# Optimization experiments

Hardware: AMD Instinct MI355X
Metric: run time of the kernel (lower is better)

The kernel has to match this reference:

```python
import jax, jax.numpy as jnp
import numpy as np

# binactive: sign() forward, straight-through (hardtanh) backward, matching the CUDA kernel
@jax.custom_vjp
def binactive(x):
    return jnp.sign(x)

def _binactive_fwd(x):
    return jnp.sign(x), x

def _binactive_bwd(x, g):
    return (g * (jnp.abs(x) <= 1.0).astype(g.dtype),)

binactive.defvjp(_binactive_fwd, _binactive_bwd)

B, C_IN, C_OUT, K, H, W = 32, 256, 256, 3, 56, 56

def setup_inputs() -> dict:
    key = jax.random.key(0)
    k1, k2, k3 = jax.random.split(key, 3)
    x = jax.random.normal(k1, (B, C_IN, H, W), dtype=jnp.float32)
    n = C_IN * (K ^ 2)  # faithful to the (buggy) `kernel_size ^ 2` in reset_parameters
    stdv = 1.0 / np.sqrt(n)
    weight = jax.random.uniform(k2, (C_OUT, C_IN, K, K), dtype=jnp.float32, minval=-stdv, maxval=stdv)
    mask = jax.random.uniform(k3, (C_OUT, 1, 1, 1), dtype=jnp.float32, minval=-1e-4, maxval=1e-4)
    return {"x": x, "weight": weight, "mask": mask}

def reference(x, weight, mask):
    xb = binactive(x)                      # sign-binarized activations, [B,Cin,H,W]
    fm = (binactive(mask) - 1.0) / 2.0     # binact=True branch: 0 if mask>0, -1 if mask<0
    w = weight * fm + weight               # per-output-filter gating of weights
    out = jax.lax.conv_general_dilated(
        xb, w,
        window_strides=(1, 1),
        padding=((1, 1), (1, 1)),
        dimension_numbers=("NCHW", "OIHW", "NCHW"),
    )
    return out  # [B, Cout, H, W]
```

## Files before the change

kernel.cpp:

```cpp
#include <hip/hip_runtime.h>

#define B_    32
#define CIN   256
#define COUT  256
#define Hh    56
#define Ww    56
#define HP    58
#define WP    58
#define Kk    2304
#define NT    18

#define QSCALE 2016.0f
#define QINV   (1.0f/2016.0f)

#define XPAD_BYTES ((size_t)B_*HP*WP*CIN)
#define XPAD_GUARD 16384
#define AWT_OFF    (XPAD_BYTES + XPAD_GUARD)
#define AWT_BYTES  ((size_t)NT*32768)
#define META_OFF   (AWT_OFF + AWT_BYTES)
#define WS_REQUIRED (META_OFF + 1040)

#define LDS_TOTAL 90112
#define TP 260

typedef __attribute__((ext_vector_type(4))) int i32x4;

__device__ __forceinline__ void gload_lds16(const void* g, void* l) {
  __builtin_amdgcn_global_load_lds(
      (const __attribute__((address_space(1))) unsigned int*)g,
      (__attribute__((address_space(3))) unsigned int*)l, 16, 0, 0);
}

__global__ __launch_bounds__(256) void prep_all(
    const float* __restrict__ x,
    const float* __restrict__ wgt,
    const float* __restrict__ mask,
    int* __restrict__ meta,
    signed char* __restrict__ awt,
    signed char* __restrict__ xp) {
  const int t = threadIdx.x;
  const int bid = blockIdx.x;
  if (bid < HP * B_) {
    const int hp = bid % HP, b = bid / HP;
    unsigned* orow = (unsigned*)(xp + (size_t)(b * HP + hp) * WP * CIN);
    if (hp == 0 || hp == HP - 1) {
      for (int i = t; i < WP * CIN / 4; i += 256) orow[i] = 0u;
      return;
    }
    __shared__ __align__(16) signed char tile[WP * TP];
    const int h = hp - 1;
    tile[t] = 0;
    tile[(WP - 1) * TP + t] = 0;
    const int tx = t & 63, ty = t >> 6;
    if (tx < Ww) {
      const float* xr = x + ((size_t)b * CIN * Hh + h) * Ww;
      for (int ci0 = ty * 4; ci0 < CIN; ci0 += 16) {
        unsigned pk = 0;
        #pragma unroll
        for (int j = 0; j < 4; ++j) {
          float xv = xr[(size_t)(ci0 + j) * (Hh * Ww) + tx];
          unsigned s = (xv > 0.f) ? 1u : (xv < 0.f ? 0xFFu : 0u);
          pk |= s << (8 * j);
        }
        *(unsigned*)&tile[(1 + tx) * TP + ci0] = pk;
      }
    }
    __syncthreads();
    for (int i = t; i < WP * CIN / 4; i += 256) {
      const int byte = i * 4;
      const int wp = byte >> 8;
      const int slot_p = (byte >> 4) & 15;
      const int slot_l = slot_p ^ (wp & 15);
      orow[i] = *(const unsigned*)&tile[wp * TP + slot_l * 16 + (byte & 15)];
    }
  } else {
    __shared__ int sc[256];
    __shared__ int sperm[256];
    const int fl = (mask[t] >= 0.0f) ? 1 : 0;
    sc[t] = fl;
    __syncthreads();
    for (int off = 1; off < 256; off <<= 1) {
      int v = sc[t];
      int u = (t >= off) ? sc[t - off] : 0;
      __syncthreads();
      sc[t] = v + u;
      __syncthreads();
    }
    const int incl = sc[t], act = sc[255];
    const int pos = fl ? (incl - 1) : (act + t - incl);
    sperm[pos] = t;
    __syncthreads();
    const int slot = bid - HP * B_;
    if (slot == 0) {
      meta[1 + pos] = t;
      if (t == 0) meta[0] = act;
    }
    const int co = sperm[slot];
    const float m = mask[co];
    const float scl = (m > 0.f ? 1.f : (m < 0.f ? 0.f : 0.5f)) * QSCALE;
    const float* wc = wgt + (size_t)co * Kk;
    for (int o = t; o < Kk; o += 256) {
      int tap = o >> 8, ci = o & 255;
      int q = __float2int_rn(wc[ci * 9 + tap] * scl);
      int kt = tap * 2 + (ci >> 7);
      int kk = ci & 127;
      awt[((size_t)kt * 2048 + (kk >> 4) * 256 + slot) * 16 + (kk & 15)] =
          (signed char)q;
    }
  }
}

__global__ __launch_bounds__(512, 2) void gemm_i8g(
    const signed char* __restrict__ xp,
    const signed char* __restrict__ awt,
    const int* __restrict__ meta,
    float* __restrict__ out) {
  extern __shared__ char smem[];

  const int t = threadIdx.x;
  const int nb = blockIdx.x, by = blockIdx.y;
  const int b = nb / 14, h0 = (nb % 14) * 4;

  const int act = meta[0];
  const int rem = act - by * 128;
  const int g64 = (rem <= 0) ? 0 : ((rem >= 128) ? 2 : ((rem + 63) >> 6));

  const int wid = t >> 6, lane = t & 63;
  const int wm = wid >> 2, wn = wid & 3;
  const int lc = lane & 15, lr = lane >> 4;

  i32x4 acc[4][4] = {};

  if (g64 > 0) {
    const signed char* xsrc = xp + ((size_t)b * HP + h0) * WP * CIN;
    char* dB = smem + t * 16;
    #pragma unroll
    for (int j = 0; j < 11; ++j)
      gload_lds16(xsrc + t * 16 + j * 8192, dB + j * 8192);
    asm volatile("s_waitcnt vmcnt(0)" ::: "memory");
    __builtin_amdgcn_sched_barrier(0);
    __builtin_amdgcn_s_barrier();
    __builtin_amdgcn_sched_barrier(0);

    const signed char* awg = awt + (size_t)(by * 128 + wm * 64 + lc) * 16;
    const bool run = (wm < g64);
    i32x4 afA[8], afB[8], bf[4];

#define LOAD_A_G(ktx, AF) do { if (run) { _Pragma("unroll")                    \
    for (int s_ = 0; s_ < 2; ++s_) { _Pragma("unroll")                         \
      for (int m_ = 0; m_ < 4; ++m_)                                           \
        AF[s_ * 4 + m_] = *(const i32x4*)(awg + (size_t)(ktx) * 32768 +        \
                                          (s_ * 4 + lr) * 4096 + m_ * 256); }  \
  } } while (0)

#define KT_COMP(ktx, AF) do { if (run) {                                       \
    const int tap_ = (ktx) >> 1;                                               \
    const int kh_ = tap_ / 3, kw_ = tap_ - kh_ * 3;                            \
    const int kbit_ = ((ktx) & 1) * 8;                                         \
    const int brow_ = ((wn + kh_) * WP) * 256;                                 \
    _Pragma("unroll")                                                          \
    for (int s_ = 0; s_ < 2; ++s_) {                                           \
      const int sl_ = kbit_ + s_ * 4 + lr;                                     \
      _Pragma("unroll")                                                        \
      for (int nf_ = 0; nf_ < 4; ++nf_) {                                      \
        const int wp_ = kw_ + nf_ * 16 + lc;                                   \
        bf[nf_] = *(const i32x4*)(smem + brow_ + wp_ * 256 +                   \
                                  ((sl_ ^ (wp_ & 15)) << 4));                  \
      }                                                                        \
      __builtin_amdgcn_s_setprio(1);                                           \
      _Pragma("unroll")                                                        \
      for (int m_ = 0; m_ < 4; ++m_) { _Pragma("unroll")                       \
        for (int n_ = 0; n_ < 4; ++n_)                                         \
          acc[m_][n_] = __builtin_amdgcn_mfma_i32_16x16x64_i8(                 \
              AF[s_ * 4 + m_], bf[n_], acc[m_][n_], 0, 0, 0); }                \
      __builtin_amdgcn_s_setprio(0);                                           \
    }                                                                          \
  } } while (0)

    LOAD_A_G(0, afA);
#pragma unroll 1
    for (int it = 0; it < NT / 2; ++it) {
      const int ka = 2 * it, kb = 2 * it + 1;
      const int kc2 = (kb + 1 < NT) ? kb + 1 : NT - 1;
      LOAD_A_G(kb, afB);
      KT_COMP(ka, afA);
      LOAD_A_G(kc2, afA);
      KT_COMP(kb, afB);
    }
  }

  const int* perm = meta + 1;
  const int h = h0 + wn;
  #pragma unroll
  for (int m = 0; m < 4; ++m) {
    const int slotb = by * 128 + wm * 64 + m * 16 + lr * 4;
    const int c0 = perm[slotb], c1 = perm[slotb + 1];
    const int c2 = perm[slotb + 2], c3 = perm[slotb + 3];
    const int cos[4] = {c0, c1, c2, c3};
    #pragma unroll
    for (int nf = 0; nf < 4; ++nf) {
      const int w = nf * 16 + lc;
      if (w < Ww) {
        #pragma unroll
        for (int r = 0; r < 4; ++r)
          out[(((size_t)b * COUT + cos[r]) * Hh + h) * Ww + w] =
              (float)acc[m][nf][r] * QINV;
      }
    }
  }
}

__global__ __launch_bounds__(256) void binconv_naive(
    const float* __restrict__ x,
    const float* __restrict__ wgt,
    const float* __restrict__ mask,
    float* __restrict__ out) {
  const int w  = threadIdx.x;
  const int h  = blockIdx.x * 4 + threadIdx.y;
  const int co = blockIdx.y;
  const int b  = blockIdx.z;

  const float m = mask[co];
  const float scale = (m > 0.f) ? 1.f : ((m < 0.f) ? 0.f : 0.5f);

  const size_t obase = (((size_t)b * COUT + co) * Hh + h) * Ww + w;
  if (scale == 0.f) {
    if (w < Ww) out[obase] = 0.f;
    return;
  }

  const float* __restrict__ xb = x   + (size_t)b  * CIN * Hh * Ww;
  const float* __restrict__ wc = wgt + (size_t)co * CIN * 9;

  float acc = 0.f;
  for (int ci = 0; ci < CIN; ++ci) {
    const float* __restrict__ xc = xb + (size_t)ci * (Hh * Ww);
    const float* __restrict__ wk = wc + ci * 9;
    float wv[9];
    #pragma unroll
    for (int t2 = 0; t2 < 9; ++t2) wv[t2] = wk[t2];
    #pragma unroll
    for (int kh = 0; kh < 3; ++kh) {
      const int hh = h + kh - 1;
      if (hh < 0 || hh >= Hh) continue;
      const float* __restrict__ xr = xc + hh * Ww;
      #pragma unroll
      for (int kw = 0; kw < 3; ++kw) {
        const int ww = w + kw - 1;
        float xv = (ww >= 0 && ww < Ww) ? xr[ww] : 0.f;
        float s = (xv > 0.f) ? 1.f : ((xv < 0.f) ? -1.f : 0.f);
        acc += s * wv[kh * 3 + kw];
      }
    }
  }
  if (w < Ww) out[obase] = acc * scale;
}

extern "C" void kernel_launch(void* const* d_in, const int* in_sizes, int n_in,
                              void* d_out, int out_size, void* d_ws, size_t ws_size,
                              hipStream_t stream) {
  const float* x    = (const float*)d_in[0];
  const float* wgt  = (const float*)d_in[1];
  const float* mask = (const float*)d_in[2];
  float* out = (float*)d_out;

  bool ok = ws_size >= WS_REQUIRED;
  if (ok) {
    hipError_t e = hipFuncSetAttribute(
        (const void*)gemm_i8g, hipFuncAttributeMaxDynamicSharedMemorySize,
        LDS_TOTAL);
    ok = (e == hipSuccess);
  }
  if (!ok) {
    hipLaunchKernelGGL(binconv_naive, dim3(Hh / 4, COUT, B_), dim3(64, 4, 1),
                       0, stream, x, wgt, mask, out);
    return;
  }

  signed char* xp8 = (signed char*)d_ws;
  signed char* awt = (signed char*)d_ws + AWT_OFF;
  int* meta        = (int*)((char*)d_ws + META_OFF);

  hipLaunchKernelGGL(prep_all, dim3(HP * B_ + 256), dim3(256), 0, stream,
                     x, wgt, mask, meta, awt, xp8);
  hipLaunchKernelGGL(gemm_i8g, dim3(448, 2), dim3(512), LDS_TOTAL, stream,
                     xp8, awt, meta, out);
}
```

Measured before the change: 76.99 us.

## Enlarge conv output tile to seven rows per block for halo and weight reuse

Each block now covers seven output rows of one image instead of four, loading a 9-row padded input slab into LDS and spreading 112 output positions per wave across rows. This amortizes the 2-row halo and the per-k-step weight fragment loads over more MFMAs. In exchange LDS use rises to about 136KB per block, likely limiting residency to one block per CU, and accumulator register pressure grows.

```diff
diff --git a/kernel.cpp b/kernel.cpp
--- a/kernel.cpp
+++ b/kernel.cpp
@@ -20,7 +20,7 @@
 #define META_OFF   (AWT_OFF + AWT_BYTES)
 #define WS_REQUIRED (META_OFF + 1040)
 
-#define LDS_TOTAL 90112
+#define LDS_TOTAL 139264
 #define TP 260
 
 typedef __attribute__((ext_vector_type(4))) int i32x4;
@@ -110,7 +110,7 @@
   }
 }
 
-__global__ __launch_bounds__(512, 2) void gemm_i8g(
+__global__ __launch_bounds__(512, 2) void gemm_i8h(
     const signed char* __restrict__ xp,
     const signed char* __restrict__ awt,
     const int* __restrict__ meta,
@@ -119,7 +119,7 @@
 
   const int t = threadIdx.x;
   const int nb = blockIdx.x, by = blockIdx.y;
-  const int b = nb / 14, h0 = (nb % 14) * 4;
+  const int b = nb >> 3, h0 = (nb & 7) * 7;
 
   const int act = meta[0];
   const int rem = act - by * 128;
@@ -129,13 +129,21 @@
   const int wm = wid >> 2, wn = wid & 3;
   const int lc = lane & 15, lr = lane >> 4;
 
-  i32x4 acc[4][4] = {};
+  i32x4 acc[4][7] = {};
+
+  int hrel_[7], wv_[7];
+  #pragma unroll
+  for (int nf = 0; nf < 7; ++nf) {
+    const int ng = wn * 112 + nf * 16 + lc;
+    hrel_[nf] = ng >> 6;
+    wv_[nf] = ng & 63;
+  }
 
   if (g64 > 0) {
     const signed char* xsrc = xp + ((size_t)b * HP + h0) * WP * CIN;
     char* dB = smem + t * 16;
     #pragma unroll
-    for (int j = 0; j < 11; ++j)
+    for (int j = 0; j < 17; ++j)
       gload_lds16(xsrc + t * 16 + j * 8192, dB + j * 8192);
     asm volatile("s_waitcnt vmcnt(0)" ::: "memory");
     __builtin_amdgcn_sched_barrier(0);
@@ -144,7 +152,7 @@
 
     const signed char* awg = awt + (size_t)(by * 128 + wm * 64 + lc) * 16;
     const bool run = (wm < g64);
-    i32x4 afA[8], afB[8], bf[4];
+    i32x4 afA[8], afB[8];
 
 #define LOAD_A_G(ktx, AF) do { if (run) { _Pragma("unroll")                    \
     for (int s_ = 0; s_ < 2; ++s_) { _Pragma("unroll")                         \
@@ -157,23 +165,22 @@
     const int tap_ = (ktx) >> 1;                                               \
     const int kh_ = tap_ / 3, kw_ = tap_ - kh_ * 3;                            \
     const int kbit_ = ((ktx) & 1) * 8;                                         \
-    const int brow_ = ((wn + kh_) * WP) * 256;                                 \
     _Pragma("unroll")                                                          \
     for (int s_ = 0; s_ < 2; ++s_) {                                           \
       const int sl_ = kbit_ + s_ * 4 + lr;                                     \
       _Pragma("unroll")                                                        \
-      for (int nf_ = 0; nf_ < 4; ++nf_) {                                      \
-        const int wp_ = kw_ + nf_ * 16 + lc;                                   \
-        bf[nf_] = *(const i32x4*)(smem + brow_ + wp_ * 256 +                   \
-                                  ((sl_ ^ (wp_ & 15)) << 4));                  \
+      for (int nf_ = 0; nf_ < 7; ++nf_) {                                      \
+        const int wp_ = kw_ + wv_[nf_];                                        \
+        const i32x4 bfv = *(const i32x4*)(smem +                               \
+            ((hrel_[nf_] + kh_) * WP + wp_) * 256 +                            \
+            ((sl_ ^ (wp_ & 15)) << 4));                                        \
+        __builtin_amdgcn_s_setprio(1);                                         \
+        _Pragma("unroll")                                                      \
+        for (int m_ = 0; m_ < 4; ++m_)                                         \
+          acc[m_][nf_] = __builtin_amdgcn_mfma_i32_16x16x64_i8(                \
+              AF[s_ * 4 + m_], bfv, acc[m_][nf_], 0, 0, 0);                    \
+        __builtin_amdgcn_s_setprio(0);                                         \
       }                                                                        \
-      __builtin_amdgcn_s_setprio(1);                                           \
-      _Pragma("unroll")                                                        \
-      for (int m_ = 0; m_ < 4; ++m_) { _Pragma("unroll")                       \
-        for (int n_ = 0; n_ < 4; ++n_)                                         \
-          acc[m_][n_] = __builtin_amdgcn_mfma_i32_16x16x64_i8(                 \
-              AF[s_ * 4 + m_], bf[n_], acc[m_][n_], 0, 0, 0); }                \
-      __builtin_amdgcn_s_setprio(0);                                           \
     }                                                                          \
   } } while (0)
 
@@ -190,7 +197,6 @@
   }
 
   const int* perm = meta + 1;
-  const int h = h0 + wn;
   #pragma unroll
   for (int m = 0; m < 4; ++m) {
     const int slotb = by * 128 + wm * 64 + m * 16 + lr * 4;
@@ -198,8 +204,9 @@
     const int c2 = perm[slotb + 2], c3 = perm[slotb + 3];
     const int cos[4] = {c0, c1, c2, c3};
     #pragma unroll
-    for (int nf = 0; nf < 4; ++nf) {
-      const int w = nf * 16 + lc;
+    for (int nf = 0; nf < 7; ++nf) {
+      const int w = wv_[nf];
+      const int h = h0 + hrel_[nf];
       if (w < Ww) {
         #pragma unroll
         for (int r = 0; r < 4; ++r)
@@ -267,7 +274,7 @@
   bool ok = ws_size >= WS_REQUIRED;
   if (ok) {
     hipError_t e = hipFuncSetAttribute(
-        (const void*)gemm_i8g, hipFuncAttributeMaxDynamicSharedMemorySize,
+        (const void*)gemm_i8h, hipFuncAttributeMaxDynamicSharedMemorySize,
         LDS_TOTAL);
     ok = (e == hipSuccess);
   }
@@ -283,6 +290,6 @@
 
   hipLaunchKernelGGL(prep_all, dim3(HP * B_ + 256), dim3(256), 0, stream,
                      x, wgt, mask, meta, awt, xp8);
-  hipLaunchKernelGGL(gemm_i8g, dim3(448, 2), dim3(512), LDS_TOTAL, stream,
+  hipLaunchKernelGGL(gemm_i8h, dim3(256, 2), dim3(512), LDS_TOTAL, stream,
                      xp8, awt, meta, out);
 }
```

New measurement: 75.12 us. -2.4%, faster.
